# Optimization experiments

Hardware: AMD Instinct MI355X
Metric: run time of the kernel (lower is better)

## Reference

```python
import jax, jax.numpy as jnp
import numpy as np

IN_CH, OUT_CH, MODES = 64, 64, 16
BATCH, N = 64, 8192


def setup_inputs() -> dict:
    key = jax.random.key(0)
    k1, k2, k3 = jax.random.split(key, 3)
    scale = 1.0 / (IN_CH * OUT_CH)
    x = jax.random.normal(k1, (BATCH, IN_CH, N), dtype=jnp.float32)
    w_real = scale * jax.random.uniform(k2, (IN_CH, OUT_CH, MODES), dtype=jnp.float32)
    w_imag = scale * jax.random.uniform(k3, (IN_CH, OUT_CH, MODES), dtype=jnp.float32)
    return {"x": x, "w_real": w_real, "w_imag": w_imag}


def reference(x, w_real, w_imag):
    # x: (b, in_ch, n) real. weights: (in_ch, out_ch, modes) complex.
    n = x.shape[-1]
    weights = w_real + 1j * w_imag                      # complex64
    x_ft = jnp.fft.rfft(x)                              # (b, in_ch, n//2+1) complex
    # multiply only the lowest `modes` frequencies by learned complex weights
    out_modes = jnp.einsum('bix,iox->box', x_ft[:, :, :MODES], weights)
    n_freq = n // 2 + 1
    out_ft = jnp.zeros((x.shape[0], OUT_CH, n_freq), dtype=jnp.complex64)
    out_ft = out_ft.at[:, :, :MODES].set(out_modes)
    return jnp.fft.irfft(out_ft, n=n)                   # (b, out_ch, n) real
```

## Files before the change

### kernel.cpp

```cpp
#include <hip/hip_runtime.h>

#define NPTS 8192


__global__ __launch_bounds__(256) void prep_kernel(const float* __restrict__ wr,
                                                   const float* __restrict__ wi,
                                                   float* __restrict__ wtr,
                                                   float* __restrict__ wti) {
    int idx = blockIdx.x * 256 + threadIdx.x;
    int i = idx >> 10, o = (idx >> 4) & 63, k = idx & 15;
    int dst = k * 4096 + i * 64 + o;
    wtr[dst] = wr[idx];
    wti[dst] = wi[idx];
}

__global__ __launch_bounds__(256) void dft_kernel(const float* __restrict__ x,
                                                  float* __restrict__ Xp) {
    __shared__ float smem[8448];
    const int t = threadIdx.x;
    const int rb = blockIdx.x >> 3, seg = blockIdx.x & 7;
    const int rowbase = rb * 16, segbase = seg * 1024;
    const int lane = t & 31, grp = t >> 5;
    const int r0 = (grp & 1) * 8;
    const int k0 = (grp >> 1) * 4;

    float2 cv[2][4], sv[2][4];
#pragma unroll
    for (int i = 0; i < 2; ++i)
#pragma unroll
        for (int j = 0; j < 4; ++j) {
            int k = k0 + j;
            int n = segbase + i * 64 + lane * 2;
            int p0 = (k * n) & 8191;
            int p1 = (k * (n + 1)) & 8191;
            cv[i][j] = make_float2(cospif(p0 * (1.0f / 4096.0f)),
                                   cospif(p1 * (1.0f / 4096.0f)));
            sv[i][j] = make_float2(sinpif(p0 * (1.0f / 4096.0f)),
                                   sinpif(p1 * (1.0f / 4096.0f)));
        }
    float cd[4], sd[4];
#pragma unroll
    for (int j = 0; j < 4; ++j) {
        cd[j] = cospif((k0 + j) * (1.0f / 32.0f));
        sd[j] = sinpif((k0 + j) * (1.0f / 32.0f));
    }

    float ar[8][4] = {{0.f}}, ai[8][4] = {{0.f}};

    float4 A[2], B[2];
#define LOADX(c, dst)                                                              \
    {                                                                              \
        _Pragma("unroll") for (int jj = 0; jj < 2; ++jj) {                         \
            int p = t + jj * 256;                                                  \
            dst[jj] = *(const float4*)&x[(rowbase + (p >> 5)) * NPTS + segbase +   \
                                         (c) * 128 + (p & 31) * 4];                \
        }                                                                          \
    }
#define COMPUTE(bufofs)                                                            \
    {                                                                              \
        const float2* xs2 = (const float2*)(smem + (bufofs));                      \
        _Pragma("unroll") for (int i = 0; i < 2; ++i) {                            \
            float2 xv[8];                                                          \
            _Pragma("unroll") for (int r = 0; r < 8; ++r)                          \
                xv[r] = xs2[(r0 + r) * 64 + i * 32 + lane];                        \
            _Pragma("unroll") for (int r = 0; r < 8; ++r)                          \
                _Pragma("unroll") for (int j = 0; j < 4; ++j) {                    \
                    ar[r][j] += xv[r].x * cv[i][j].x + xv[r].y * cv[i][j].y;       \
                    ai[r][j] -= xv[r].x * sv[i][j].x + xv[r].y * sv[i][j].y;       \
                }                                                                  \
        }                                                                          \
    }
#define ROTATE()                                                                   \
    {                                                                              \
        _Pragma("unroll") for (int i = 0; i < 2; ++i)                              \
            _Pragma("unroll") for (int j = 0; j < 4; ++j) {                        \
                float cx = cv[i][j].x * cd[j] - sv[i][j].x * sd[j];                \
                float sx = sv[i][j].x * cd[j] + cv[i][j].x * sd[j];                \
                float cy = cv[i][j].y * cd[j] - sv[i][j].y * sd[j];                \
                float sy = sv[i][j].y * cd[j] + cv[i][j].y * sd[j];                \
                cv[i][j] = make_float2(cx, cy);                                    \
                sv[i][j] = make_float2(sx, sy);                                    \
            }                                                                      \
    }

    LOADX(0, A)
    LOADX(1, B)
    for (int ch = 0; ch < 8; ch += 2) {
        __syncthreads();
        ((float4*)smem)[t] = A[0];
        ((float4*)smem)[t + 256] = A[1];
        if (ch + 2 < 8) LOADX(ch + 2, A)
        __syncthreads();
        COMPUTE(0)
        ROTATE()
        __syncthreads();
        ((float4*)(smem + 2048))[t] = B[0];
        ((float4*)(smem + 2048))[t + 256] = B[1];
        if (ch + 3 < 8) LOADX(ch + 3, B)
        __syncthreads();
        COMPUTE(2048)
        ROTATE()
    }

    __syncthreads();
#pragma unroll
    for (int r = 0; r < 8; ++r)
#pragma unroll
        for (int j = 0; j < 4; ++j)
            smem[grp * 1056 + (r * 4 + j) * 33 + lane] = ar[r][j];
    __syncthreads();
    {
        float s = 0.f;
#pragma unroll
        for (int l = 0; l < 32; ++l) s += smem[grp * 1056 + lane * 33 + l];
        int r = lane >> 2, j = lane & 3;
        int row = rowbase + (grp & 1) * 8 + r;
        int k = (grp >> 1) * 4 + j;
        Xp[((seg * 16 + k) * 2 + 0) * 4096 + row] = s;
    }
    __syncthreads();
#pragma unroll
    for (int r = 0; r < 8; ++r)
#pragma unroll
        for (int j = 0; j < 4; ++j)
            smem[grp * 1056 + (r * 4 + j) * 33 + lane] = ai[r][j];
    __syncthreads();
    {
        float s = 0.f;
#pragma unroll
        for (int l = 0; l < 32; ++l) s += smem[grp * 1056 + lane * 33 + l];
        int r = lane >> 2, j = lane & 3;
        int row = rowbase + (grp & 1) * 8 + r;
        int k = (grp >> 1) * 4 + j;
        Xp[((seg * 16 + k) * 2 + 1) * 4096 + row] = s;
    }
#undef LOADX
#undef COMPUTE
#undef ROTATE
}

__global__ __launch_bounds__(256) void mix_kernel(const float* __restrict__ Xp,
                                                  const float* __restrict__ wtr,
                                                  const float* __restrict__ wti,
                                                  float* __restrict__ yc) {
    __shared__ float xre[16 * 65], xim[16 * 65];
    __shared__ float wlr[4096], wli[4096];
    const int t = threadIdx.x;
    const int k = blockIdx.x & 15, bq = blockIdx.x >> 4;
#pragma unroll
    for (int j = 0; j < 4; ++j) {
        int lr = t + j * 256;
        int row = bq * 1024 + lr;
        float re = 0.f, im = 0.f;
#pragma unroll
        for (int s = 0; s < 8; ++s) {
            re += Xp[((s * 16 + k) * 2 + 0) * 4096 + row];
            im += Xp[((s * 16 + k) * 2 + 1) * 4096 + row];
        }
        xre[(lr >> 6) * 65 + (lr & 63)] = re;
        xim[(lr >> 6) * 65 + (lr & 63)] = im;
        ((float4*)wlr)[t + j * 256] = ((const float4*)(wtr + k * 4096))[t + j * 256];
        ((float4*)wli)[t + j * 256] = ((const float4*)(wti + k * 4096))[t + j * 256];
    }
    __syncthreads();
    const int bt = t >> 4;
    const int o4 = t & 15;
    float accr[4] = {0.f, 0.f, 0.f, 0.f}, acci[4] = {0.f, 0.f, 0.f, 0.f};
    for (int i = 0; i < 64; ++i) {
        float xr = xre[bt * 65 + i], xi = xim[bt * 65 + i];
        float4 w4r = ((const float4*)wlr)[i * 16 + o4];
        float4 w4i = ((const float4*)wli)[i * 16 + o4];
        accr[0] += xr * w4r.x - xi * w4i.x;  acci[0] += xr * w4i.x + xi * w4r.x;
        accr[1] += xr * w4r.y - xi * w4i.y;  acci[1] += xr * w4i.y + xi * w4r.y;
        accr[2] += xr * w4r.z - xi * w4i.z;  acci[2] += xr * w4i.z + xi * w4r.z;
        accr[3] += xr * w4r.w - xi * w4i.w;  acci[3] += xr * w4i.w + xi * w4r.w;
    }
    const float invn = 1.0f / 8192.0f;
#pragma unroll
    for (int oo = 0; oo < 4; ++oo) {
        int row = (bq * 16 + bt) * 64 + o4 * 4 + oo;
        if (k == 0) {
            yc[row * 32]      = accr[oo] * invn;
            yc[row * 32 + 16] = 0.f;
        } else {
            yc[row * 32 + k]      = 2.f * accr[oo] * invn;
            yc[row * 32 + 16 + k] = -2.f * acci[oo] * invn;
        }
    }
}

__global__ __launch_bounds__(256) void synth_kernel(const float* __restrict__ yc,
                                                    float* __restrict__ out) {
    __shared__ float cf[512];
    const int t = threadIdx.x;
    const int rg = blockIdx.x >> 4, tile = blockIdx.x & 15;
    cf[t]       = yc[rg * 512 + t];
    cf[t + 256] = yc[rg * 512 + 256 + t];

    const int n0 = tile * 512 + t * 2;
    float2 cb[16], sb[16];
    cb[0] = make_float2(1.f, 1.f);
    sb[0] = make_float2(0.f, 0.f);
    {
        float a0 = (float)(n0 & 8191) * (1.0f / 4096.0f);
        float a1 = (float)((n0 + 1) & 8191) * (1.0f / 4096.0f);
        cb[1] = make_float2(cospif(a0), cospif(a1));
        sb[1] = make_float2(sinpif(a0), sinpif(a1));
    }
#pragma unroll
    for (int k = 2; k < 16; ++k) {
        cb[k] = make_float2(cb[k-1].x * cb[1].x - sb[k-1].x * sb[1].x,
                            cb[k-1].y * cb[1].y - sb[k-1].y * sb[1].y);
        sb[k] = make_float2(sb[k-1].x * cb[1].x + cb[k-1].x * sb[1].x,
                            sb[k-1].y * cb[1].y + cb[k-1].y * sb[1].y);
    }
    __syncthreads();
#pragma unroll 4
    for (int r = 0; r < 16; ++r) {
        const float4* c4 = (const float4*)&cf[r * 32];
        float ax = 0.f, ay = 0.f;
#pragma unroll
        for (int j = 0; j < 4; ++j) {
            float4 a = c4[j];
            float4 s = c4[4 + j];
            ax += a.x * cb[4*j].x + a.y * cb[4*j+1].x + a.z * cb[4*j+2].x + a.w * cb[4*j+3].x
                + s.x * sb[4*j].x + s.y * sb[4*j+1].x + s.z * sb[4*j+2].x + s.w * sb[4*j+3].x;
            ay += a.x * cb[4*j].y + a.y * cb[4*j+1].y + a.z * cb[4*j+2].y + a.w * cb[4*j+3].y
                + s.x * sb[4*j].y + s.y * sb[4*j+1].y + s.z * sb[4*j+2].y + s.w * sb[4*j+3].y;
        }
        *(float2*)&out[(rg * 16 + r) * NPTS + n0] = make_float2(ax, ay);
    }
}

extern "C" void kernel_launch(void* const* d_in, const int* in_sizes, int n_in,
                              void* d_out, int out_size, void* d_ws, size_t ws_size,
                              hipStream_t stream) {
    const float* x  = (const float*)d_in[0];
    const float* wr = (const float*)d_in[1];
    const float* wi = (const float*)d_in[2];
    float* out = (float*)d_out;
    float* ws  = (float*)d_ws;
    float* yc  = ws;
    float* wtr = ws + 131072;
    float* wti = ws + 196608;
    float* Xp  = out;

    prep_kernel<<<256, 256, 0, stream>>>(wr, wi, wtr, wti);
    dft_kernel<<<2048, 256, 0, stream>>>(x, Xp);
    mix_kernel<<<64, 256, 0, stream>>>(Xp, wtr, wti, yc);
    synth_kernel<<<4096, 256, 0, stream>>>(yc, out);
}
```

Baseline: 310.3 us.

## Compute forward DFT with split-bf16 MFMA against precomputed twiddle basis

Replaces the scalar FMA forward DFT, which used rotating twiddles and an LDS reduction, with MFMA 16x16x32 bf16 matrix multiplies. Both x and a precomputed cos/sin basis are split into high and low bf16 parts, and three MFMA products approximate fp32 accuracy. The prep kernel now also builds the basis table in scratch space inside the output buffer. Segments per row go from 8 to 16, and mix_kernel sums 16 partials instead of 8. The change trades extra basis memory traffic and reduced precision for tensor-core throughput.

```diff
diff --git a/kernel.cpp b/kernel.cpp
--- a/kernel.cpp
+++ b/kernel.cpp
@@ -1,142 +1,115 @@
 #include <hip/hip_runtime.h>
 
 #define NPTS 8192
+
+typedef __bf16 bf16x8 __attribute__((ext_vector_type(8)));
+typedef short short8 __attribute__((ext_vector_type(8)));
+typedef float f32x4 __attribute__((ext_vector_type(4)));
 
 
 __global__ __launch_bounds__(256) void prep_kernel(const float* __restrict__ wr,
                                                    const float* __restrict__ wi,
                                                    float* __restrict__ wtr,
-                                                   float* __restrict__ wti) {
-    int idx = blockIdx.x * 256 + threadIdx.x;
-    int i = idx >> 10, o = (idx >> 4) & 63, k = idx & 15;
-    int dst = k * 4096 + i * 64 + o;
-    wtr[dst] = wr[idx];
-    wti[dst] = wi[idx];
+                                                   float* __restrict__ wti,
+                                                   ushort* __restrict__ bas) {
+    const int bid = blockIdx.x, t = threadIdx.x;
+    if (bid < 256) {
+        int idx = bid * 256 + t;
+        int i = idx >> 10, o = (idx >> 4) & 63, k = idx & 15;
+        int dst = k * 4096 + i * 64 + o;
+        wtr[dst] = wr[idx];
+        wti[dst] = wi[idx];
+    } else {
+        int e = (bid - 256) * 256 + t;
+        int j = e & 7;
+        int lane = (e >> 3) & 63;
+        int gk = (e >> 9) & 255;
+        int ct = e >> 17;
+        int m = lane & 15;
+        int n = gk * 32 + ((lane >> 4) & 3) * 8 + j;
+        int p = (m * n) & 8191;
+        float a = (float)p * (1.0f / 4096.0f);
+        float v = ct ? -sinpif(a) : cospif(a);
+        unsigned u = __float_as_uint(v);
+        unsigned hb = (u + 0x7fffu + ((u >> 16) & 1u)) >> 16;
+        float hf = __uint_as_float(hb << 16);
+        float lo = v - hf;
+        unsigned ul = __float_as_uint(lo);
+        unsigned lb = (ul + 0x7fffu + ((ul >> 16) & 1u)) >> 16;
+        bas[e] = (ushort)hb;
+        bas[262144 + e] = (ushort)lb;
+    }
 }
 
 __global__ __launch_bounds__(256) void dft_kernel(const float* __restrict__ x,
+                                                  const ushort* __restrict__ bas,
                                                   float* __restrict__ Xp) {
-    __shared__ float smem[8448];
     const int t = threadIdx.x;
-    const int rb = blockIdx.x >> 3, seg = blockIdx.x & 7;
-    const int rowbase = rb * 16, segbase = seg * 1024;
-    const int lane = t & 31, grp = t >> 5;
-    const int r0 = (grp & 1) * 8;
-    const int k0 = (grp >> 1) * 4;
-
-    float2 cv[2][4], sv[2][4];
-#pragma unroll
-    for (int i = 0; i < 2; ++i)
-#pragma unroll
-        for (int j = 0; j < 4; ++j) {
-            int k = k0 + j;
-            int n = segbase + i * 64 + lane * 2;
-            int p0 = (k * n) & 8191;
-            int p1 = (k * (n + 1)) & 8191;
-            cv[i][j] = make_float2(cospif(p0 * (1.0f / 4096.0f)),
-                                   cospif(p1 * (1.0f / 4096.0f)));
-            sv[i][j] = make_float2(sinpif(p0 * (1.0f / 4096.0f)),
-                                   sinpif(p1 * (1.0f / 4096.0f)));
-        }
-    float cd[4], sd[4];
-#pragma unroll
-    for (int j = 0; j < 4; ++j) {
-        cd[j] = cospif((k0 + j) * (1.0f / 32.0f));
-        sd[j] = sinpif((k0 + j) * (1.0f / 32.0f));
-    }
-
-    float ar[8][4] = {{0.f}}, ai[8][4] = {{0.f}};
-
-    float4 A[2], B[2];
-#define LOADX(c, dst)                                                              \
-    {                                                                              \
-        _Pragma("unroll") for (int jj = 0; jj < 2; ++jj) {                         \
-            int p = t + jj * 256;                                                  \
-            dst[jj] = *(const float4*)&x[(rowbase + (p >> 5)) * NPTS + segbase +   \
-                                         (c) * 128 + (p & 31) * 4];                \
-        }                                                                          \
-    }
-#define COMPUTE(bufofs)                                                            \
-    {                                                                              \
-        const float2* xs2 = (const float2*)(smem + (bufofs));                      \
-        _Pragma("unroll") for (int i = 0; i < 2; ++i) {                            \
-            float2 xv[8];                                                          \
-            _Pragma("unroll") for (int r = 0; r < 8; ++r)                          \
-                xv[r] = xs2[(r0 + r) * 64 + i * 32 + lane];                        \
-            _Pragma("unroll") for (int r = 0; r < 8; ++r)                          \
-                _Pragma("unroll") for (int j = 0; j < 4; ++j) {                    \
-                    ar[r][j] += xv[r].x * cv[i][j].x + xv[r].y * cv[i][j].y;       \
-                    ai[r][j] -= xv[r].x * sv[i][j].x + xv[r].y * sv[i][j].y;       \
-                }                                                                  \
-        }                                                                          \
-    }
-#define ROTATE()                                                                   \
-    {                                                                              \
-        _Pragma("unroll") for (int i = 0; i < 2; ++i)                              \
-            _Pragma("unroll") for (int j = 0; j < 4; ++j) {                        \
-                float cx = cv[i][j].x * cd[j] - sv[i][j].x * sd[j];                \
-                float sx = sv[i][j].x * cd[j] + cv[i][j].x * sd[j];                \
-                float cy = cv[i][j].y * cd[j] - sv[i][j].y * sd[j];                \
-                float sy = sv[i][j].y * cd[j] + cv[i][j].y * sd[j];                \
-                cv[i][j] = make_float2(cx, cy);                                    \
-                sv[i][j] = make_float2(sx, sy);                                    \
-            }                                                                      \
-    }
-
-    LOADX(0, A)
-    LOADX(1, B)
-    for (int ch = 0; ch < 8; ch += 2) {
-        __syncthreads();
-        ((float4*)smem)[t] = A[0];
-        ((float4*)smem)[t + 256] = A[1];
-        if (ch + 2 < 8) LOADX(ch + 2, A)
-        __syncthreads();
-        COMPUTE(0)
-        ROTATE()
-        __syncthreads();
-        ((float4*)(smem + 2048))[t] = B[0];
-        ((float4*)(smem + 2048))[t + 256] = B[1];
-        if (ch + 3 < 8) LOADX(ch + 3, B)
-        __syncthreads();
-        COMPUTE(2048)
-        ROTATE()
-    }
-
-    __syncthreads();
-#pragma unroll
-    for (int r = 0; r < 8; ++r)
-#pragma unroll
-        for (int j = 0; j < 4; ++j)
-            smem[grp * 1056 + (r * 4 + j) * 33 + lane] = ar[r][j];
-    __syncthreads();
-    {
-        float s = 0.f;
-#pragma unroll
-        for (int l = 0; l < 32; ++l) s += smem[grp * 1056 + lane * 33 + l];
-        int r = lane >> 2, j = lane & 3;
-        int row = rowbase + (grp & 1) * 8 + r;
-        int k = (grp >> 1) * 4 + j;
-        Xp[((seg * 16 + k) * 2 + 0) * 4096 + row] = s;
-    }
-    __syncthreads();
-#pragma unroll
-    for (int r = 0; r < 8; ++r)
-#pragma unroll
-        for (int j = 0; j < 4; ++j)
-            smem[grp * 1056 + (r * 4 + j) * 33 + lane] = ai[r][j];
-    __syncthreads();
-    {
-        float s = 0.f;
-#pragma unroll
-        for (int l = 0; l < 32; ++l) s += smem[grp * 1056 + lane * 33 + l];
-        int r = lane >> 2, j = lane & 3;
-        int row = rowbase + (grp & 1) * 8 + r;
-        int k = (grp >> 1) * 4 + j;
-        Xp[((seg * 16 + k) * 2 + 1) * 4096 + row] = s;
-    }
-#undef LOADX
-#undef COMPUTE
-#undef ROTATE
+    const int lane = t & 63, w = t >> 6;
+    const int rb = blockIdx.x >> 4, seg = blockIdx.x & 15;
+    const int rowq = lane >> 4;
+    const int row = rb * 64 + w * 16 + (lane & 15);
+    const float* xp = x + (size_t)row * NPTS + seg * 512 + rowq * 8;
+    const bf16x8* bh = (const bf16x8*)bas;
+    const bf16x8* bl = (const bf16x8*)(bas + 262144);
+    const int gk0 = seg * 16;
+
+    f32x4 acc0 = {0.f, 0.f, 0.f, 0.f};
+    f32x4 acc1 = {0.f, 0.f, 0.f, 0.f};
+
+    float4 xa = *(const float4*)xp;
+    float4 xb = *(const float4*)(xp + 4);
+    bf16x8 c0h = bh[gk0 * 64 + lane];
+    bf16x8 c1h = bh[(256 + gk0) * 64 + lane];
+    bf16x8 c0l = bl[gk0 * 64 + lane];
+    bf16x8 c1l = bl[(256 + gk0) * 64 + lane];
+
+    for (int ks = 0; ks < 16; ++ks) {
+        short8 hsv, lsv;
+        {
+            float v[8] = {xa.x, xa.y, xa.z, xa.w, xb.x, xb.y, xb.z, xb.w};
+#pragma unroll
+            for (int j = 0; j < 8; ++j) {
+                unsigned u = __float_as_uint(v[j]);
+                hsv[j] = (short)(u >> 16);
+                float lo = v[j] - __uint_as_float(u & 0xffff0000u);
+                unsigned ul = __float_as_uint(lo);
+                lsv[j] = (short)((ul + 0x7fffu + ((ul >> 16) & 1u)) >> 16);
+            }
+        }
+        bf16x8 ah = __builtin_bit_cast(bf16x8, hsv);
+        bf16x8 al = __builtin_bit_cast(bf16x8, lsv);
+
+        float4 nxa, nxb;
+        bf16x8 n0h, n1h, n0l, n1l;
+        if (ks < 15) {
+            const float* xq = xp + (ks + 1) * 32;
+            nxa = *(const float4*)xq;
+            nxb = *(const float4*)(xq + 4);
+            int gk = gk0 + ks + 1;
+            n0h = bh[gk * 64 + lane];
+            n1h = bh[(256 + gk) * 64 + lane];
+            n0l = bl[gk * 64 + lane];
+            n1l = bl[(256 + gk) * 64 + lane];
+        }
+
+        acc0 = __builtin_amdgcn_mfma_f32_16x16x32_bf16(ah, c0h, acc0, 0, 0, 0);
+        acc1 = __builtin_amdgcn_mfma_f32_16x16x32_bf16(ah, c1h, acc1, 0, 0, 0);
+        acc0 = __builtin_amdgcn_mfma_f32_16x16x32_bf16(al, c0h, acc0, 0, 0, 0);
+        acc1 = __builtin_amdgcn_mfma_f32_16x16x32_bf16(al, c1h, acc1, 0, 0, 0);
+        acc0 = __builtin_amdgcn_mfma_f32_16x16x32_bf16(ah, c0l, acc0, 0, 0, 0);
+        acc1 = __builtin_amdgcn_mfma_f32_16x16x32_bf16(ah, c1l, acc1, 0, 0, 0);
+
+        if (ks < 15) {
+            xa = nxa; xb = nxb;
+            c0h = n0h; c1h = n1h; c0l = n0l; c1l = n1l;
+        }
+    }
+
+    const int k = lane & 15;
+    const int rbase = rb * 64 + w * 16 + rowq * 4;
+    *(f32x4*)&Xp[(size_t)((seg * 16 + k) * 2 + 0) * 4096 + rbase] = acc0;
+    *(f32x4*)&Xp[(size_t)((seg * 16 + k) * 2 + 1) * 4096 + rbase] = acc1;
 }
 
 __global__ __launch_bounds__(256) void mix_kernel(const float* __restrict__ Xp,
@@ -153,7 +126,7 @@
         int row = bq * 1024 + lr;
         float re = 0.f, im = 0.f;
 #pragma unroll
-        for (int s = 0; s < 8; ++s) {
+        for (int s = 0; s < 16; ++s) {
             re += Xp[((s * 16 + k) * 2 + 0) * 4096 + row];
             im += Xp[((s * 16 + k) * 2 + 1) * 4096 + row];
         }
@@ -244,9 +217,10 @@
     float* wtr = ws + 131072;
     float* wti = ws + 196608;
     float* Xp  = out;
-
-    prep_kernel<<<256, 256, 0, stream>>>(wr, wi, wtr, wti);
-    dft_kernel<<<2048, 256, 0, stream>>>(x, Xp);
+    ushort* bas = (ushort*)(out + 2097152);
+
+    prep_kernel<<<1280, 256, 0, stream>>>(wr, wi, wtr, wti, bas);
+    dft_kernel<<<1024, 256, 0, stream>>>(x, bas, Xp);
     mix_kernel<<<64, 256, 0, stream>>>(Xp, wtr, wti, yc);
     synth_kernel<<<4096, 256, 0, stream>>>(yc, out);
 }
```

Result: faster. 282.3 us (-9.0%).
